# Kernel optimization log

Measured on AMD Instinct MI355X. Metric: run time of the kernel, lower is better.

## Reference

```python
import jax, jax.numpy as jnp
import numpy as np

B, N, D_IN, HID = 8, 2048, 256, 64  # batch, nodes, input hidden, graph hidden (heads=1)
NEG_INF = -9e15  # matches -9000000000000000.0 in the torch code


def setup_inputs() -> dict:
    key = jax.random.key(0)
    k1, k2, k3, k4 = jax.random.split(key, 4)
    node_features = jax.random.normal(k1, (B, N, D_IN), dtype=jnp.float32)
    adj = jax.random.randint(k2, (B, N, N), 0, 2, dtype=jnp.int32)
    W = jax.random.normal(k3, (D_IN, HID), dtype=jnp.float32) / np.sqrt(D_IN).astype(np.float32)
    a = jax.random.normal(k4, (2 * HID, 1), dtype=jnp.float32) * 0.1
    return {"node_features": node_features, "adj": adj, "W": W, "a": a}


def reference(node_features, adj, W, a):
    # Wh = W(node_features): (B, N, HID)
    Wh = jnp.einsum('bnd,dh->bnh', node_features, W)
    a1 = a[:HID, 0]   # attention vector for the 'source' half of the concat
    a2 = a[HID:, 0]   # attention vector for the 'neighbor' half
    f1 = Wh @ a1      # (B, N) = Wh_i . a1
    f2 = Wh @ a2      # (B, N) = Wh_j . a2
    # e_ij = leakyrelu([Wh_i || Wh_j] . a) -- avoids the O(N^2 * 2*HID) concat
    e = jax.nn.leaky_relu(f1[:, :, None] + f2[:, None, :], negative_slope=0.2)  # (B, N, N)
    att = jnp.where(adj > 0, e, jnp.float32(NEG_INF))
    att = jax.nn.softmax(att, axis=2)
    # dropout is identity in eval / with graph_dropout=0.0
    h_prime = jnp.einsum('bij,bjh->bih', att, Wh)  # (B, N, HID)
    return h_prime
```

## Files before the change

kernel.cpp:

```cpp
#include <hip/hip_runtime.h>

#define NB 8
#define NN 2048
#define DIN 256
#define HID 64
#define JSPLIT 8

typedef _Float16 f16x8_t __attribute__((ext_vector_type(8)));
typedef float f32x16_t __attribute__((ext_vector_type(16)));

__global__ __launch_bounds__(256) void k_prep(
    const float* __restrict__ x, const float* __restrict__ W,
    const float* __restrict__ a, const int* __restrict__ adj,
    unsigned long long* __restrict__ mb, _Float16* __restrict__ wht,
    float* __restrict__ f1, float* __restrict__ f2)
{
    __shared__ float smem[DIN * 64];
    const int bid = blockIdx.x;
    const int t = threadIdx.x;

    if (bid >= 256) {
        const int lane = t & 63;
        const int wave = (bid - 256) * 4 + (t >> 6);
#pragma unroll
        for (int rr = 0; rr < 2; ++rr) {
            const int row = wave * 2 + rr;
            const int* ar = adj + (size_t)row * NN;
            unsigned long long myw = 0;
#pragma unroll
            for (int k = 0; k < 32; ++k) {
                unsigned long long bal = __ballot(ar[k * 64 + lane] != 0);
                if ((lane & 31) == k) myw = bal;
            }
            if (lane < 32) mb[(size_t)row * 32 + lane] = myw;
        }
        return;
    }

    const int g0 = bid * 64;
    const int b = g0 >> 11;
    const int n0 = g0 & (NN - 1);

    const float4* x4 = (const float4*)x;
#pragma unroll
    for (int it = 0; it < 16; ++it) {
        int c = t + it * 256;
        int row = c & 63;
        int dg = c >> 6;
        float4 v = x4[(size_t)(g0 + row) * 64 + dg];
        smem[(dg * 4 + 0) * 64 + row] = v.x;
        smem[(dg * 4 + 1) * 64 + row] = v.y;
        smem[(dg * 4 + 2) * 64 + row] = v.z;
        smem[(dg * 4 + 3) * 64 + row] = v.w;
    }
    __syncthreads();

    const int hq = t & 15;
    const int rg = t >> 4;
    const float4* W4 = (const float4*)W;
    float acc[4][4] = {};
#pragma unroll 8
    for (int d = 0; d < DIN; ++d) {
        float4 wv = W4[d * 16 + hq];
        float4 xv = *(const float4*)&smem[d * 64 + rg * 4];
        float xr[4] = {xv.x, xv.y, xv.z, xv.w};
        float wk[4] = {wv.x, wv.y, wv.z, wv.w};
#pragma unroll
        for (int r = 0; r < 4; ++r)
#pragma unroll
            for (int k = 0; k < 4; ++k) acc[r][k] += xr[r] * wk[k];
    }

    float4 a1v = ((const float4*)a)[hq];
    float4 a2v = ((const float4*)a)[16 + hq];
#pragma unroll
    for (int r = 0; r < 4; ++r) {
        float p1 = acc[r][0] * a1v.x + acc[r][1] * a1v.y + acc[r][2] * a1v.z + acc[r][3] * a1v.w;
        float p2 = acc[r][0] * a2v.x + acc[r][1] * a2v.y + acc[r][2] * a2v.z + acc[r][3] * a2v.w;
#pragma unroll
        for (int m = 1; m < 16; m <<= 1) {
            p1 += __shfl_xor(p1, m);
            p2 += __shfl_xor(p2, m);
        }
        if (hq == 0) {
            f1[g0 + rg * 4 + r] = p1;
            f2[g0 + rg * 4 + r] = p2;
        }
    }

    __syncthreads();
#pragma unroll
    for (int r = 0; r < 4; ++r)
#pragma unroll
        for (int k = 0; k < 4; ++k) {
            int h = hq * 4 + k;
            int row = rg * 4 + r;
            smem[h * 64 + (((row >> 2) ^ (h & 15)) << 2) + (row & 3)] = acc[r][k];
        }
    __syncthreads();

    const int h = t >> 2;
    const int rc = t & 3;
    union { _Float16 fh[16]; uint4 u4[2]; } uh;
#pragma unroll
    for (int q = 0; q < 4; ++q) {
        float4 v = *(const float4*)&smem[h * 64 + (((rc * 4 + q) ^ (h & 15)) << 2)];
        uh.fh[q * 4 + 0] = (_Float16)v.x;
        uh.fh[q * 4 + 1] = (_Float16)v.y;
        uh.fh[q * 4 + 2] = (_Float16)v.z;
        uh.fh[q * 4 + 3] = (_Float16)v.w;
    }
    size_t obase = (size_t)(b * HID + h) * NN + n0 + rc * 16;
    *(uint4*)&wht[obase] = uh.u4[0];
    *(uint4*)&wht[obase + 8] = uh.u4[1];
}

__global__ __launch_bounds__(256) void k_f2max(
    const float* __restrict__ f2, float* __restrict__ f2mx)
{
    __shared__ float red[4];
    const int b = blockIdx.x, t = threadIdx.x;
    float m = -3.4e38f;
    for (int i = t; i < NN; i += 256) m = fmaxf(m, f2[b * NN + i]);
#pragma unroll
    for (int s = 1; s < 64; s <<= 1) m = fmaxf(m, __shfl_xor(m, s));
    if ((t & 63) == 0) red[t >> 6] = m;
    __syncthreads();
    if (t == 0) f2mx[b] = fmaxf(fmaxf(red[0], red[1]), fmaxf(red[2], red[3]));
}

__global__ __launch_bounds__(256, 4) void k_attn(
    const unsigned long long* __restrict__ mb, const _Float16* __restrict__ wht,
    const float* __restrict__ f1, const float* __restrict__ f2,
    const float* __restrict__ f2mx,
    float* __restrict__ accp, float* __restrict__ zp)
{
    __shared__ _Float16 whx[64 * 128];
    const int t = threadIdx.x;
    const int w = t >> 6, lane = t & 63;
    const int bx = blockIdx.x;
    const int js = bx & 7;
    const int it = (bx >> 3) & 15;
    const int b = bx >> 7;
    const int I0 = it * 128 + w * 32;
    const int half = lane >> 5;
    const int m32 = lane & 31;
    const int row = I0 + m32;
    const int jb0 = js * 256;

    const float f1v = f1[b * NN + row];
    float Mi = f1v + f2mx[b];
    Mi = Mi > 0.f ? Mi : 0.2f * Mi;
    const float LOG2E = 1.4426950408889634f;
    const float negMiL = -Mi * LOG2E;
    const float* f2p = f2 + b * NN;

    const unsigned long long* mrow = mb + (size_t)(b * NN + row) * 32 + js * 4;
    unsigned long long m[4];
    {
        ulonglong2 q0 = *(const ulonglong2*)mrow;
        ulonglong2 q1 = *(const ulonglong2*)(mrow + 2);
        m[0] = q0.x; m[1] = q0.y; m[2] = q1.x; m[3] = q1.y;
    }

    f32x16_t acc0, acc1;
#pragma unroll
    for (int i = 0; i < 16; ++i) { acc0[i] = 0.f; acc1[i] = 0.f; }
    float zacc = 0.f;

#pragma unroll
    for (int stg = 0; stg < 2; ++stg) {
        const int jt = jb0 + stg * 128;
        if (stg) __syncthreads();
#pragma unroll
        for (int cc = 0; cc < 4; ++cc) {
            int c = t + cc * 256;
            int h = c >> 4, g = c & 15;
            int gp = g ^ (h & 15);
            size_t src = (size_t)(b * HID + h) * NN + jt + g * 8;
            *(uint4*)&whx[h * 128 + gp * 8] = *(const uint4*)&wht[src];
        }
        __syncthreads();
#pragma unroll
        for (int s8 = 0; s8 < 8; ++s8) {
            const int jl = jt + s8 * 16 + half * 8;
            const uint32_t bits8 =
                (uint32_t)(m[stg * 2 + (s8 >> 2)] >> (((s8 & 3) * 16) + half * 8)) & 0xffu;
            float4 fa = *(const float4*)&f2p[jl];
            float4 fb = *(const float4*)&f2p[jl + 4];
            float fv[8] = {fa.x, fa.y, fa.z, fa.w, fb.x, fb.y, fb.z, fb.w};
            f16x8_t ah;
#pragma unroll
            for (int jj = 0; jj < 8; ++jj) {
                float t1 = f1v + fv[jj];
                t1 = fmaxf(t1, 0.2f * t1);
                float pv = (bits8 & (1u << jj))
                         ? __builtin_amdgcn_exp2f(fmaf(t1, LOG2E, negMiL))
                         : 0.f;
                _Float16 ph = (_Float16)pv;
                ah[jj] = ph;
                zacc += (float)ph;
            }
            const int gx = (2 * s8 + half) ^ (m32 & 15);
            f16x8_t b0 = *(const f16x8_t*)&whx[m32 * 128 + (gx << 3)];
            f16x8_t b1 = *(const f16x8_t*)&whx[(m32 + 32) * 128 + (gx << 3)];
            acc0 = __builtin_amdgcn_mfma_f32_32x32x16_f16(ah, b0, acc0, 0, 0, 0);
            acc1 = __builtin_amdgcn_mfma_f32_32x32x16_f16(ah, b1, acc1, 0, 0, 0);
        }
    }

    float zrow = zacc + __shfl_xor(zacc, 32);
    if (lane < 32) zp[(size_t)(js * NB + b) * NN + row] = zrow;
    float* ap = accp + (size_t)(js * NB + b) * NN * HID;
#pragma unroll
    for (int r = 0; r < 16; ++r) {
        int rr = (r & 3) + 8 * (r >> 2) + 4 * half;
        ap[(size_t)(I0 + rr) * HID + m32] = acc0[r];
        ap[(size_t)(I0 + rr) * HID + m32 + 32] = acc1[r];
    }
}

__global__ __launch_bounds__(256) void k_combine(
    const float* __restrict__ accp, const float* __restrict__ zp,
    float* __restrict__ out)
{
    int gid = blockIdx.x * 256 + threadIdx.x;
    int h4 = gid & 15;
    int rowg = gid >> 4;
    float z = 0.f;
    float sx = 0.f, sy = 0.f, sz = 0.f, sw = 0.f;
#pragma unroll
    for (int js = 0; js < JSPLIT; ++js) {
        size_t base = (size_t)js * NB * NN;
        z += zp[base + rowg];
        float4 v = ((const float4*)accp)[(base + rowg) * 16 + h4];
        sx += v.x; sy += v.y; sz += v.z; sw += v.w;
    }
    float zi = 1.f / z;
    float4 o = {sx * zi, sy * zi, sz * zi, sw * zi};
    ((float4*)out)[gid] = o;
}

extern "C" void kernel_launch(void* const* d_in, const int* in_sizes, int n_in,
                              void* d_out, int out_size, void* d_ws, size_t ws_size,
                              hipStream_t stream)
{
    const float* x = (const float*)d_in[0];
    const int* adj = (const int*)d_in[1];
    const float* W = (const float*)d_in[2];
    const float* a = (const float*)d_in[3];
    float* out = (float*)d_out;
    char* ws = (char*)d_ws;

    _Float16* wht = (_Float16*)(ws);
    float* f1   = (float*)(ws + (2u << 20));
    float* f2   = (float*)(ws + (2u << 20) + (64u << 10));
    float* f2mx = (float*)(ws + (2u << 20) + (128u << 10));
    unsigned long long* mbuf = (unsigned long long*)(ws + (3u << 20));
    float* accp = (float*)(ws + (8u << 20));
    float* zp   = (float*)(ws + (40u << 20));

    hipLaunchKernelGGL(k_prep, dim3(2304), dim3(256), 0, stream,
                       x, W, a, adj, mbuf, wht, f1, f2);
    hipLaunchKernelGGL(k_f2max, dim3(NB), dim3(256), 0, stream, f2, f2mx);
    hipLaunchKernelGGL(k_attn, dim3(1024), dim3(256), 0, stream, mbuf, wht, f1, f2, f2mx, accp, zp);
    hipLaunchKernelGGL(k_combine, dim3(1024), dim3(256), 0, stream, accp, zp, out);
}
```

Measured before the change: 235.5 us.

## Store split-K partials in fp16, compute row sums via MFMA, pack conversions

The attention kernel now writes its per-split partial accumulators as fp16 instead of fp32, halving the partial buffer traffic into and out of the combine kernel. The softmax denominator is computed with an extra MFMA against a ones vector instead of per-lane scalar adds and a shuffle, and probability conversion uses packed round-toward-zero cvt. This adds a third MFMA per step and loses precision in the stored partials, which may risk fp16 overflow or rounding.

```diff
diff --git a/kernel.cpp b/kernel.cpp
--- a/kernel.cpp
+++ b/kernel.cpp
@@ -7,6 +7,8 @@
 #define JSPLIT 8
 
 typedef _Float16 f16x8_t __attribute__((ext_vector_type(8)));
+typedef _Float16 f16x2_t __attribute__((ext_vector_type(2)));
+typedef _Float16 f16x4_t __attribute__((ext_vector_type(4)));
 typedef float f32x16_t __attribute__((ext_vector_type(16)));
 
 __global__ __launch_bounds__(256) void k_prep(
@@ -133,7 +135,7 @@
     const unsigned long long* __restrict__ mb, const _Float16* __restrict__ wht,
     const float* __restrict__ f1, const float* __restrict__ f2,
     const float* __restrict__ f2mx,
-    float* __restrict__ accp, float* __restrict__ zp)
+    _Float16* __restrict__ accp, float* __restrict__ zp)
 {
     __shared__ _Float16 whx[64 * 128];
     const int t = threadIdx.x;
@@ -163,10 +165,13 @@
         m[0] = q0.x; m[1] = q0.y; m[2] = q1.x; m[3] = q1.y;
     }
 
-    f32x16_t acc0, acc1;
-#pragma unroll
-    for (int i = 0; i < 16; ++i) { acc0[i] = 0.f; acc1[i] = 0.f; }
-    float zacc = 0.f;
+    f16x8_t bones;
+#pragma unroll
+    for (int i = 0; i < 8; ++i) bones[i] = (_Float16)1.0f;
+
+    f32x16_t acc0, acc1, acc2;
+#pragma unroll
+    for (int i = 0; i < 16; ++i) { acc0[i] = 0.f; acc1[i] = 0.f; acc2[i] = 0.f; }
 
 #pragma unroll
     for (int stg = 0; stg < 2; ++stg) {
@@ -189,55 +194,60 @@
             float4 fa = *(const float4*)&f2p[jl];
             float4 fb = *(const float4*)&f2p[jl + 4];
             float fv[8] = {fa.x, fa.y, fa.z, fa.w, fb.x, fb.y, fb.z, fb.w};
-            f16x8_t ah;
-#pragma unroll
-            for (int jj = 0; jj < 8; ++jj) {
-                float t1 = f1v + fv[jj];
-                t1 = fmaxf(t1, 0.2f * t1);
-                float pv = (bits8 & (1u << jj))
-                         ? __builtin_amdgcn_exp2f(fmaf(t1, LOG2E, negMiL))
-                         : 0.f;
-                _Float16 ph = (_Float16)pv;
-                ah[jj] = ph;
-                zacc += (float)ph;
+            union { f16x2_t h2[4]; f16x8_t v; } ua;
+#pragma unroll
+            for (int jp = 0; jp < 4; ++jp) {
+                float pv[2];
+#pragma unroll
+                for (int e = 0; e < 2; ++e) {
+                    int jj = jp * 2 + e;
+                    float t1 = f1v + fv[jj];
+                    t1 = fmaxf(t1, 0.2f * t1);
+                    pv[e] = (bits8 & (1u << jj))
+                          ? __builtin_amdgcn_exp2f(fmaf(t1, LOG2E, negMiL))
+                          : 0.f;
+                }
+                auto pk = __builtin_amdgcn_cvt_pkrtz(pv[0], pv[1]);
+                ua.h2[jp] = *(f16x2_t*)&pk;
             }
             const int gx = (2 * s8 + half) ^ (m32 & 15);
             f16x8_t b0 = *(const f16x8_t*)&whx[m32 * 128 + (gx << 3)];
             f16x8_t b1 = *(const f16x8_t*)&whx[(m32 + 32) * 128 + (gx << 3)];
-            acc0 = __builtin_amdgcn_mfma_f32_32x32x16_f16(ah, b0, acc0, 0, 0, 0);
-            acc1 = __builtin_amdgcn_mfma_f32_32x32x16_f16(ah, b1, acc1, 0, 0, 0);
-        }
-    }
-
-    float zrow = zacc + __shfl_xor(zacc, 32);
-    if (lane < 32) zp[(size_t)(js * NB + b) * NN + row] = zrow;
-    float* ap = accp + (size_t)(js * NB + b) * NN * HID;
+            acc0 = __builtin_amdgcn_mfma_f32_32x32x16_f16(ua.v, b0, acc0, 0, 0, 0);
+            acc1 = __builtin_amdgcn_mfma_f32_32x32x16_f16(ua.v, b1, acc1, 0, 0, 0);
+            acc2 = __builtin_amdgcn_mfma_f32_32x32x16_f16(ua.v, bones, acc2, 0, 0, 0);
+        }
+    }
+
+    float* zb = zp + (size_t)(js * NB + b) * NN;
+    _Float16* ap = accp + (size_t)(js * NB + b) * NN * HID;
 #pragma unroll
     for (int r = 0; r < 16; ++r) {
         int rr = (r & 3) + 8 * (r >> 2) + 4 * half;
-        ap[(size_t)(I0 + rr) * HID + m32] = acc0[r];
-        ap[(size_t)(I0 + rr) * HID + m32 + 32] = acc1[r];
+        if (m32 == 0) zb[I0 + rr] = acc2[r];
+        ap[(size_t)(I0 + rr) * HID + m32] = (_Float16)acc0[r];
+        ap[(size_t)(I0 + rr) * HID + m32 + 32] = (_Float16)acc1[r];
     }
 }
 
 __global__ __launch_bounds__(256) void k_combine(
-    const float* __restrict__ accp, const float* __restrict__ zp,
+    const _Float16* __restrict__ accp, const float* __restrict__ zp,
     float* __restrict__ out)
 {
     int gid = blockIdx.x * 256 + threadIdx.x;
     int h4 = gid & 15;
     int rowg = gid >> 4;
     float z = 0.f;
-    float sx = 0.f, sy = 0.f, sz = 0.f, sw = 0.f;
+    float s0 = 0.f, s1 = 0.f, s2 = 0.f, s3 = 0.f;
 #pragma unroll
     for (int js = 0; js < JSPLIT; ++js) {
         size_t base = (size_t)js * NB * NN;
         z += zp[base + rowg];
-        float4 v = ((const float4*)accp)[(base + rowg) * 16 + h4];
-        sx += v.x; sy += v.y; sz += v.z; sw += v.w;
+        f16x4_t v = *(const f16x4_t*)&accp[(base + rowg) * HID + h4 * 4];
+        s0 += (float)v[0]; s1 += (float)v[1]; s2 += (float)v[2]; s3 += (float)v[3];
     }
     float zi = 1.f / z;
-    float4 o = {sx * zi, sy * zi, sz * zi, sw * zi};
+    float4 o = {s0 * zi, s1 * zi, s2 * zi, s3 * zi};
     ((float4*)out)[gid] = o;
 }
 
@@ -257,8 +267,8 @@
     float* f2   = (float*)(ws + (2u << 20) + (64u << 10));
     float* f2mx = (float*)(ws + (2u << 20) + (128u << 10));
     unsigned long long* mbuf = (unsigned long long*)(ws + (3u << 20));
-    float* accp = (float*)(ws + (8u << 20));
-    float* zp   = (float*)(ws + (40u << 20));
+    _Float16* accp = (_Float16*)(ws + (8u << 20));
+    float* zp   = (float*)(ws + (24u << 20));
 
     hipLaunchKernelGGL(k_prep, dim3(2304), dim3(256), 0, stream,
                        x, W, a, adj, mbuf, wht, f1, f2);
```

After: 227.1 us. 1.04x faster.
